# Kernel optimization log

Hardware: AMD Instinct MI355X
Metric: run time of the kernel (lower is better)

The kernel has to match this reference:

```python
import jax, jax.numpy as jnp
import numpy as np

N_HEAD = 12

def fillnan(x):
    return jnp.nan_to_num(x, nan=0.0, posinf=0.0, neginf=0.0)

def setup_inputs() -> dict:
    key = jax.random.key(0)
    k1, k2, k3 = jax.random.split(key, 3)
    B, T, C = 2, 2048, 768
    x = jax.random.normal(k1, (B, T, C), dtype=jnp.float32)
    W_attn = jax.random.normal(k2, (3 * C, C), dtype=jnp.float32) * 0.02
    W_proj = jax.random.normal(k3, (C, C), dtype=jnp.float32) * 0.02
    return {"x": x, "W_attn": W_attn, "W_proj": W_proj}

def reference(x, W_attn, W_proj):
    B, T, C = x.shape
    H = N_HEAD
    D = C // H
    # qkv projection (torch Linear: x @ W^T), then nan-sanitize
    qkv = fillnan(jnp.einsum('btc,fc->btf', x, W_attn))  # [B,T,3C]
    q, k, v = jnp.split(qkv, 3, axis=-1)
    # [B,T,C] -> [B,H,T,D]
    q = q.reshape(B, T, H, D).transpose(0, 2, 1, 3)
    k = k.reshape(B, T, H, D).transpose(0, 2, 1, 3)
    v = v.reshape(B, T, H, D).transpose(0, 2, 1, 3)
    scale = 1.0 / np.sqrt(D).astype(np.float32)
    att = jnp.einsum('bhqd,bhkd->bhqk', q, k) * scale  # [B,H,T,T]
    att = fillnan(att)
    causal = jnp.tril(jnp.ones((T, T), dtype=bool))
    att = jnp.where(causal[None, None], att, -jnp.inf)
    att = jax.nn.softmax(att, axis=-1)
    att = fillnan(att)
    y = jnp.einsum('bhqk,bhkd->bhqd', att, v)  # [B,H,T,D]
    y = fillnan(y)
    y = y.transpose(0, 2, 1, 3).reshape(B, T, C)
    y = fillnan(jnp.einsum('btc,fc->btf', y, W_proj))
    return y
```

## Files before the change

### kernel.cpp

```cpp
#include <hip/hip_runtime.h>

typedef __attribute__((ext_vector_type(8))) short bf16x8;
typedef __attribute__((ext_vector_type(4))) float f32x4;

__device__ __forceinline__ unsigned short f2b(float f) {
  union { float f; unsigned u; } v; v.f = f;
  return (unsigned short)((v.u + 0x7FFFu + ((v.u >> 16) & 1u)) >> 16);
}
__device__ __forceinline__ unsigned short f2b_fast(float f) {
  union { float f; unsigned u; } v; v.f = f;
  return (unsigned short)((v.u + 0x8000u) >> 16);
}

#define XN4   786432
#define WAN4  442368
#define WPN4  147456
__global__ void cvt_all(const float* __restrict__ x, const float* __restrict__ Wa,
                        const float* __restrict__ Wp,
                        unsigned short* __restrict__ xb, unsigned short* __restrict__ Wab,
                        unsigned short* __restrict__ Wpb) {
  int i = blockIdx.x * 256 + threadIdx.x;
  const float* src; unsigned short* dst; int off;
  if (i < XN4)            { src = x;  dst = xb;  off = i; }
  else if (i < XN4 + WAN4){ src = Wa; dst = Wab; off = i - XN4; }
  else                    { src = Wp; dst = Wpb; off = i - XN4 - WAN4; }
  float4 f = reinterpret_cast<const float4*>(src)[off];
  ushort4 o;
  o.x = f2b(f.x); o.y = f2b(f.y); o.z = f2b(f.z); o.w = f2b(f.w);
  reinterpret_cast<ushort4*>(dst)[off] = o;
}

#define BM 128
#define BN 128
#define BK 64

__global__ __launch_bounds__(256, 2)
void gemm_nt(const unsigned short* __restrict__ A,
             const unsigned short* __restrict__ Bm,
             int M, int N, int K, int mode,
             unsigned short* __restrict__ qb,
             unsigned short* __restrict__ kb_,
             unsigned short* __restrict__ vt,
             float* __restrict__ outf) {
  __shared__ unsigned short As[BM * BK];
  __shared__ unsigned short Bs[BN * BK];
  int tid = threadIdx.x;
  int wave = tid >> 6, lane = tid & 63;
  int quad = lane >> 4, l16 = lane & 15;
  int m0 = blockIdx.x * BM, n0 = blockIdx.y * BN;
  int wm = (wave & 1) * 64, wn = (wave >> 1) * 64;

  int srow = lane >> 3;
  int scol = ((lane & 7) ^ srow) << 3;

  f32x4 acc[4][4] = {};

  for (int k0 = 0; k0 < K; k0 += BK) {
    __syncthreads();
#pragma unroll
    for (int i = 0; i < 4; ++i) {
      int r = wave * 32 + i * 8;
      __builtin_amdgcn_global_load_lds(
          (const __attribute__((address_space(1))) unsigned int*)(A + (size_t)(m0 + r + srow) * K + k0 + scol),
          (__attribute__((address_space(3))) unsigned int*)(As + r * BK), 16, 0, 0);
      __builtin_amdgcn_global_load_lds(
          (const __attribute__((address_space(1))) unsigned int*)(Bm + (size_t)(n0 + r + srow) * K + k0 + scol),
          (__attribute__((address_space(3))) unsigned int*)(Bs + r * BK), 16, 0, 0);
    }
    __syncthreads();
#pragma unroll
    for (int kb = 0; kb < 2; ++kb) {
      int ch = (((kb << 2) | quad) ^ (l16 & 7)) << 3;
      bf16x8 af[4], bf[4];
#pragma unroll
      for (int i = 0; i < 4; ++i)
        af[i] = *reinterpret_cast<const bf16x8*>(As + (wm + i * 16 + l16) * BK + ch);
#pragma unroll
      for (int j = 0; j < 4; ++j)
        bf[j] = *reinterpret_cast<const bf16x8*>(Bs + (wn + j * 16 + l16) * BK + ch);
#pragma unroll
      for (int i = 0; i < 4; ++i)
#pragma unroll
        for (int j = 0; j < 4; ++j)
          acc[i][j] = __builtin_amdgcn_mfma_f32_16x16x32_bf16(af[i], bf[j], acc[i][j], 0, 0, 0);
    }
  }

  const float scale2 = 0.125f * 1.44269504089f;
#pragma unroll
  for (int i = 0; i < 4; ++i) {
    int mbase = m0 + wm + i * 16 + quad * 4;
#pragma unroll
    for (int j = 0; j < 4; ++j) {
      int f = n0 + wn + j * 16 + l16;
#pragma unroll
      for (int r = 0; r < 4; ++r) {
        float c = acc[i][j][r];
        int m = mbase + r;
        if (mode == 0) {
          int b = m >> 11, t = m & 2047;
          int which = f / 768;
          int f2 = f - which * 768;
          int h = f2 >> 6, d = f2 & 63;
          int bh = b * 12 + h;
          if (which == 0)      qb[((size_t)(bh * 2048 + t)) * 64 + d] = f2b(c * scale2);
          else if (which == 1) kb_[((size_t)(bh * 2048 + t)) * 64 + d] = f2b(c);
          else                 vt[((size_t)(bh * 64 + d)) * 2048 + t] = f2b(c);
        } else {
          outf[(size_t)m * N + f] = c;
        }
      }
    }
  }
}

#define PLDP 72

__global__ __launch_bounds__(256, 4)
void attn_part(const unsigned short* __restrict__ Qb,
               const unsigned short* __restrict__ Kb,
               const unsigned short* __restrict__ Vt,
               float* __restrict__ Oacc, float* __restrict__ Lacc) {
  __shared__ unsigned short Ks[64 * 64];
  __shared__ unsigned short Vs[64 * 64];
  __shared__ unsigned short P[4 * 32 * PLDP];
  const int T = 2048, D = 64;
  int wave = threadIdx.x >> 6, lane = threadIdx.x & 63;
  int quad = lane >> 4, l16 = lane & 15;

  int w = blockIdx.x;
  int bh = w / 72;
  int r = w - bh * 72;
  int b = 0;
#pragma unroll
  for (int i = 0; i < 16; ++i) {
    int nb = (i >> 1) + 1;
    if (r >= nb) { r -= nb; b = i + 1; } else break;
  }
  int c = r;
  int q0 = b * 128;
  int qrow = q0 + wave * 32;
  int kbeg = c * 256;
  int kend = kbeg + 256; if (kend > q0 + 128) kend = q0 + 128;

  const unsigned short* Qp = Qb + (size_t)bh * T * D;
  const unsigned short* Kp = Kb + (size_t)bh * T * D;
  const unsigned short* Vp = Vt + (size_t)bh * D * T;
  unsigned short* Pw = P + wave * 32 * PLDP;

  int srow = lane >> 3;
  int scol = ((lane & 7) ^ srow) << 3;

  bf16x8 aq[2][2];
#pragma unroll
  for (int qi = 0; qi < 2; ++qi)
#pragma unroll
    for (int cc = 0; cc < 2; ++cc)
      aq[qi][cc] = *reinterpret_cast<const bf16x8*>(
          Qp + (qrow + qi * 16 + l16) * D + cc * 32 + quad * 8);

  bf16x8 ones;
#pragma unroll
  for (int e = 0; e < 8; ++e) ones[e] = (short)0x3F80;

  f32x4 o[2][4] = {};
  f32x4 lacc[2] = {};

  for (int k0 = kbeg; k0 < kend; k0 += 64) {
    __syncthreads();
#pragma unroll
    for (int i = 0; i < 2; ++i) {
      int rr = wave * 16 + i * 8;
      __builtin_amdgcn_global_load_lds(
          (const __attribute__((address_space(1))) unsigned int*)(Kp + (size_t)(k0 + rr + srow) * D + scol),
          (__attribute__((address_space(3))) unsigned int*)(Ks + rr * 64), 16, 0, 0);
      __builtin_amdgcn_global_load_lds(
          (const __attribute__((address_space(1))) unsigned int*)(Vp + (size_t)(rr + srow) * T + k0 + scol),
          (__attribute__((address_space(3))) unsigned int*)(Vs + rr * 64), 16, 0, 0);
    }
    __syncthreads();

    if (k0 > qrow + 31) continue;

    f32x4 sacc[2][4] = {};
#pragma unroll
    for (int nt = 0; nt < 4; ++nt) {
      bf16x8 bk0 = *reinterpret_cast<const bf16x8*>(Ks + (nt * 16 + l16) * 64 + ((quad ^ (l16 & 7)) << 3));
      bf16x8 bk1 = *reinterpret_cast<const bf16x8*>(Ks + (nt * 16 + l16) * 64 + (((4 | quad) ^ (l16 & 7)) << 3));
#pragma unroll
      for (int qi = 0; qi < 2; ++qi) {
        sacc[qi][nt] = __builtin_amdgcn_mfma_f32_16x16x32_bf16(aq[qi][0], bk0, sacc[qi][nt], 0, 0, 0);
        sacc[qi][nt] = __builtin_amdgcn_mfma_f32_16x16x32_bf16(aq[qi][1], bk1, sacc[qi][nt], 0, 0, 0);
      }
    }

    if (k0 + 63 > qrow) {
#pragma unroll
      for (int qi = 0; qi < 2; ++qi)
#pragma unroll
        for (int nt = 0; nt < 4; ++nt) {
          int col = k0 + nt * 16 + l16;
#pragma unroll
          for (int rr = 0; rr < 4; ++rr) {
            int row = qrow + qi * 16 + quad * 4 + rr;
            sacc[qi][nt][rr] = (col <= row) ? sacc[qi][nt][rr] : -1e30f;
          }
        }
    }
#pragma unroll
    for (int qi = 0; qi < 2; ++qi)
#pragma unroll
      for (int nt = 0; nt < 4; ++nt)
#pragma unroll
        for (int rr = 0; rr < 4; ++rr)
          sacc[qi][nt][rr] = exp2f(sacc[qi][nt][rr]);

#pragma unroll
    for (int qi = 0; qi < 2; ++qi)
#pragma unroll
      for (int nt = 0; nt < 4; ++nt)
#pragma unroll
        for (int rr = 0; rr < 4; ++rr)
          Pw[(qi * 16 + quad * 4 + rr) * PLDP + nt * 16 + l16] = f2b_fast(sacc[qi][nt][rr]);
    __asm__ volatile("s_waitcnt lgkmcnt(0)" ::: "memory");

    bf16x8 vf[4][2];
#pragma unroll
    for (int dt = 0; dt < 4; ++dt) {
      vf[dt][0] = *reinterpret_cast<const bf16x8*>(Vs + (dt * 16 + l16) * 64 + ((quad ^ (l16 & 7)) << 3));
      vf[dt][1] = *reinterpret_cast<const bf16x8*>(Vs + (dt * 16 + l16) * 64 + (((4 | quad) ^ (l16 & 7)) << 3));
    }
#pragma unroll
    for (int qi = 0; qi < 2; ++qi) {
      bf16x8 ap0 = *reinterpret_cast<const bf16x8*>(Pw + (qi * 16 + l16) * PLDP + quad * 8);
      bf16x8 ap1 = *reinterpret_cast<const bf16x8*>(Pw + (qi * 16 + l16) * PLDP + 32 + quad * 8);
#pragma unroll
      for (int dt = 0; dt < 4; ++dt) {
        o[qi][dt] = __builtin_amdgcn_mfma_f32_16x16x32_bf16(ap0, vf[dt][0], o[qi][dt], 0, 0, 0);
        o[qi][dt] = __builtin_amdgcn_mfma_f32_16x16x32_bf16(ap1, vf[dt][1], o[qi][dt], 0, 0, 0);
      }
      lacc[qi] = __builtin_amdgcn_mfma_f32_16x16x32_bf16(ap0, ones, lacc[qi], 0, 0, 0);
      lacc[qi] = __builtin_amdgcn_mfma_f32_16x16x32_bf16(ap1, ones, lacc[qi], 0, 0, 0);
    }
  }

#pragma unroll
  for (int qi = 0; qi < 2; ++qi)
#pragma unroll
    for (int dt = 0; dt < 4; ++dt)
#pragma unroll
      for (int rr = 0; rr < 4; ++rr) {
        int row = qrow + qi * 16 + quad * 4 + rr;
        atomicAdd(&Oacc[((size_t)(bh * T + row)) * 64 + dt * 16 + l16], o[qi][dt][rr]);
      }
  if (l16 == 0) {
#pragma unroll
    for (int qi = 0; qi < 2; ++qi)
#pragma unroll
      for (int rr = 0; rr < 4; ++rr)
        atomicAdd(&Lacc[bh * T + qrow + qi * 16 + quad * 4 + rr], lacc[qi][rr]);
  }
}

__global__ __launch_bounds__(256)
void attn_norm(const float* __restrict__ Oacc, const float* __restrict__ Lacc,
               unsigned short* __restrict__ Yb) {
  int g = blockIdx.x * 256 + threadIdx.x;
  int d4 = g & 15;
  int t = (g >> 4) & 2047;
  int bh = g >> 15;
  int b = bh / 12, h = bh - b * 12;
  float4 ov = reinterpret_cast<const float4*>(Oacc)[g];
  float rl = 1.0f / Lacc[bh * 2048 + t];
  ushort4 y;
  y.x = f2b(ov.x * rl); y.y = f2b(ov.y * rl);
  y.z = f2b(ov.z * rl); y.w = f2b(ov.w * rl);
  *reinterpret_cast<ushort4*>(Yb + ((size_t)(b * 2048 + t)) * 768 + h * 64 + d4 * 4) = y;
}

extern "C" void kernel_launch(void* const* d_in, const int* in_sizes, int n_in,
                              void* d_out, int out_size, void* d_ws, size_t ws_size,
                              hipStream_t stream) {
  const float* x  = (const float*)d_in[0];
  const float* Wa = (const float*)d_in[1];
  const float* Wp = (const float*)d_in[2];
  float* out = (float*)d_out;

  unsigned short* ws = (unsigned short*)d_ws;
  unsigned short* xb  = ws;
  unsigned short* Wab = xb  + 3145728;
  unsigned short* Wpb = Wab + 1769472;
  unsigned short* Qb  = Wpb + 589824;
  unsigned short* Kb  = Qb  + 3145728;
  unsigned short* Vt  = Kb  + 3145728;
  unsigned short* Yb  = Vt  + 3145728;
  float*          Oacc = (float*)(Yb + 3145728);
  float*          Lacc = Oacc + 3145728;

  hipMemsetAsync(Oacc, 0, (3145728 + 49152) * sizeof(float), stream);

  cvt_all<<<(XN4 + WAN4 + WPN4) / 256, 256, 0, stream>>>(x, Wa, Wp, xb, Wab, Wpb);

  gemm_nt<<<dim3(4096 / BM, 2304 / BN), 256, 0, stream>>>(
      xb, Wab, 4096, 2304, 768, 0, Qb, Kb, Vt, nullptr);

  attn_part<<<1728, 256, 0, stream>>>(Qb, Kb, Vt, Oacc, Lacc);
  attn_norm<<<786432 / 256, 256, 0, stream>>>(Oacc, Lacc, Yb);

  gemm_nt<<<dim3(4096 / BM, 768 / BN), 256, 0, stream>>>(
      Yb, Wpb, 4096, 768, 768, 1, nullptr, nullptr, nullptr, out);
}
```

Measured before the change: 178.8 us.

## Replace split-K attention with per-query-block kernel, double-buffered KV and fused normalization

Each block now handles one 128-row query block across the full causal key range for a head. The old design split keys across blocks, accumulated partials with atomics into fp32 buffers and then ran a separate normalize kernel. K/V tiles are double-buffered in LDS so the next tile's loads overlap compute, and MFMA sections get raised wave priority. This removes the memset, the atomics and the extra kernel launch, but the grid shrinks to 384 blocks with unbalanced causal work (scheduled heaviest first) and occupancy drops to 2 blocks per CU.

```diff
diff --git a/kernel.cpp b/kernel.cpp
--- a/kernel.cpp
+++ b/kernel.cpp
@@ -116,32 +116,23 @@
 
 #define PLDP 72
 
-__global__ __launch_bounds__(256, 4)
+__global__ __launch_bounds__(256, 2)
 void attn_part(const unsigned short* __restrict__ Qb,
                const unsigned short* __restrict__ Kb,
                const unsigned short* __restrict__ Vt,
-               float* __restrict__ Oacc, float* __restrict__ Lacc) {
-  __shared__ unsigned short Ks[64 * 64];
-  __shared__ unsigned short Vs[64 * 64];
+               unsigned short* __restrict__ Yb) {
+  __shared__ unsigned short Ks[2][64 * 64];
+  __shared__ unsigned short Vs[2][64 * 64];
   __shared__ unsigned short P[4 * 32 * PLDP];
   const int T = 2048, D = 64;
   int wave = threadIdx.x >> 6, lane = threadIdx.x & 63;
   int quad = lane >> 4, l16 = lane & 15;
 
-  int w = blockIdx.x;
-  int bh = w / 72;
-  int r = w - bh * 72;
-  int b = 0;
-#pragma unroll
-  for (int i = 0; i < 16; ++i) {
-    int nb = (i >> 1) + 1;
-    if (r >= nb) { r -= nb; b = i + 1; } else break;
-  }
-  int c = r;
-  int q0 = b * 128;
+  int bh = blockIdx.x % 24;
+  int qb = 15 - blockIdx.x / 24;
+  int q0 = qb * 128;
   int qrow = q0 + wave * 32;
-  int kbeg = c * 256;
-  int kend = kbeg + 256; if (kend > q0 + 128) kend = q0 + 128;
+  int nt = 2 * qb + 2;
 
   const unsigned short* Qp = Qb + (size_t)bh * T * D;
   const unsigned short* Kp = Kb + (size_t)bh * T * D;
@@ -166,116 +157,113 @@
   f32x4 o[2][4] = {};
   f32x4 lacc[2] = {};
 
-  for (int k0 = kbeg; k0 < kend; k0 += 64) {
-    __syncthreads();
-#pragma unroll
-    for (int i = 0; i < 2; ++i) {
-      int rr = wave * 16 + i * 8;
-      __builtin_amdgcn_global_load_lds(
-          (const __attribute__((address_space(1))) unsigned int*)(Kp + (size_t)(k0 + rr + srow) * D + scol),
-          (__attribute__((address_space(3))) unsigned int*)(Ks + rr * 64), 16, 0, 0);
-      __builtin_amdgcn_global_load_lds(
-          (const __attribute__((address_space(1))) unsigned int*)(Vp + (size_t)(rr + srow) * T + k0 + scol),
-          (__attribute__((address_space(3))) unsigned int*)(Vs + rr * 64), 16, 0, 0);
-    }
-    __syncthreads();
-
-    if (k0 > qrow + 31) continue;
-
-    f32x4 sacc[2][4] = {};
-#pragma unroll
-    for (int nt = 0; nt < 4; ++nt) {
-      bf16x8 bk0 = *reinterpret_cast<const bf16x8*>(Ks + (nt * 16 + l16) * 64 + ((quad ^ (l16 & 7)) << 3));
-      bf16x8 bk1 = *reinterpret_cast<const bf16x8*>(Ks + (nt * 16 + l16) * 64 + (((4 | quad) ^ (l16 & 7)) << 3));
+#define STAGE_KV(buf, k0s)                                                          \
+  {                                                                                 \
+    _Pragma("unroll")                                                               \
+    for (int i_ = 0; i_ < 2; ++i_) {                                                \
+      int rr_ = wave * 16 + i_ * 8;                                                 \
+      __builtin_amdgcn_global_load_lds(                                             \
+          (const __attribute__((address_space(1))) unsigned int*)(Kp + (size_t)((k0s) + rr_ + srow) * 64 + scol), \
+          (__attribute__((address_space(3))) unsigned int*)(&Ks[buf][rr_ * 64]), 16, 0, 0); \
+      __builtin_amdgcn_global_load_lds(                                             \
+          (const __attribute__((address_space(1))) unsigned int*)(Vp + (size_t)(rr_ + srow) * 2048 + (k0s) + scol), \
+          (__attribute__((address_space(3))) unsigned int*)(&Vs[buf][rr_ * 64]), 16, 0, 0); \
+    }                                                                               \
+  }
+
+  STAGE_KV(0, 0);
+  asm volatile("s_waitcnt vmcnt(0)" ::: "memory");
+  __builtin_amdgcn_s_barrier();
+
+  int cur = 0;
+  for (int t = 0; t < nt; ++t) {
+    int k0 = t << 6;
+    if (t + 1 < nt) STAGE_KV(cur ^ 1, (t + 1) << 6);
+
+    if (k0 <= qrow + 31) {
+      f32x4 sacc[2][4] = {};
+      __builtin_amdgcn_s_setprio(1);
+#pragma unroll
+      for (int nt2 = 0; nt2 < 4; ++nt2) {
+        bf16x8 bk0 = *reinterpret_cast<const bf16x8*>(Ks[cur] + (nt2 * 16 + l16) * 64 + ((quad ^ (l16 & 7)) << 3));
+        bf16x8 bk1 = *reinterpret_cast<const bf16x8*>(Ks[cur] + (nt2 * 16 + l16) * 64 + (((4 | quad) ^ (l16 & 7)) << 3));
+#pragma unroll
+        for (int qi = 0; qi < 2; ++qi) {
+          sacc[qi][nt2] = __builtin_amdgcn_mfma_f32_16x16x32_bf16(aq[qi][0], bk0, sacc[qi][nt2], 0, 0, 0);
+          sacc[qi][nt2] = __builtin_amdgcn_mfma_f32_16x16x32_bf16(aq[qi][1], bk1, sacc[qi][nt2], 0, 0, 0);
+        }
+      }
+      __builtin_amdgcn_s_setprio(0);
+
+      if (k0 + 63 > qrow) {
+#pragma unroll
+        for (int qi = 0; qi < 2; ++qi)
+#pragma unroll
+          for (int nt2 = 0; nt2 < 4; ++nt2) {
+            int col = k0 + nt2 * 16 + l16;
+#pragma unroll
+            for (int rr = 0; rr < 4; ++rr) {
+              int row = qrow + qi * 16 + quad * 4 + rr;
+              sacc[qi][nt2][rr] = (col <= row) ? sacc[qi][nt2][rr] : -1e30f;
+            }
+          }
+      }
+#pragma unroll
+      for (int qi = 0; qi < 2; ++qi)
+#pragma unroll
+        for (int nt2 = 0; nt2 < 4; ++nt2)
+#pragma unroll
+          for (int rr = 0; rr < 4; ++rr)
+            sacc[qi][nt2][rr] = exp2f(sacc[qi][nt2][rr]);
+
+#pragma unroll
+      for (int qi = 0; qi < 2; ++qi)
+#pragma unroll
+        for (int nt2 = 0; nt2 < 4; ++nt2)
+#pragma unroll
+          for (int rr = 0; rr < 4; ++rr)
+            Pw[(qi * 16 + quad * 4 + rr) * PLDP + nt2 * 16 + l16] = f2b_fast(sacc[qi][nt2][rr]);
+      __asm__ volatile("s_waitcnt lgkmcnt(0)" ::: "memory");
+
+      bf16x8 vf[4][2];
+#pragma unroll
+      for (int dt = 0; dt < 4; ++dt) {
+        vf[dt][0] = *reinterpret_cast<const bf16x8*>(Vs[cur] + (dt * 16 + l16) * 64 + ((quad ^ (l16 & 7)) << 3));
+        vf[dt][1] = *reinterpret_cast<const bf16x8*>(Vs[cur] + (dt * 16 + l16) * 64 + (((4 | quad) ^ (l16 & 7)) << 3));
+      }
+      __builtin_amdgcn_s_setprio(1);
 #pragma unroll
       for (int qi = 0; qi < 2; ++qi) {
-        sacc[qi][nt] = __builtin_amdgcn_mfma_f32_16x16x32_bf16(aq[qi][0], bk0, sacc[qi][nt], 0, 0, 0);
-        sacc[qi][nt] = __builtin_amdgcn_mfma_f32_16x16x32_bf16(aq[qi][1], bk1, sacc[qi][nt], 0, 0, 0);
-      }
-    }
-
-    if (k0 + 63 > qrow) {
-#pragma unroll
-      for (int qi = 0; qi < 2; ++qi)
-#pragma unroll
-        for (int nt = 0; nt < 4; ++nt) {
-          int col = k0 + nt * 16 + l16;
-#pragma unroll
-          for (int rr = 0; rr < 4; ++rr) {
-            int row = qrow + qi * 16 + quad * 4 + rr;
-            sacc[qi][nt][rr] = (col <= row) ? sacc[qi][nt][rr] : -1e30f;
-          }
+        bf16x8 ap0 = *reinterpret_cast<const bf16x8*>(Pw + (qi * 16 + l16) * PLDP + quad * 8);
+        bf16x8 ap1 = *reinterpret_cast<const bf16x8*>(Pw + (qi * 16 + l16) * PLDP + 32 + quad * 8);
+#pragma unroll
+        for (int dt = 0; dt < 4; ++dt) {
+          o[qi][dt] = __builtin_amdgcn_mfma_f32_16x16x32_bf16(ap0, vf[dt][0], o[qi][dt], 0, 0, 0);
+          o[qi][dt] = __builtin_amdgcn_mfma_f32_16x16x32_bf16(ap1, vf[dt][1], o[qi][dt], 0, 0, 0);
         }
-    }
-#pragma unroll
-    for (int qi = 0; qi < 2; ++qi)
-#pragma unroll
-      for (int nt = 0; nt < 4; ++nt)
-#pragma unroll
-        for (int rr = 0; rr < 4; ++rr)
-          sacc[qi][nt][rr] = exp2f(sacc[qi][nt][rr]);
-
-#pragma unroll
-    for (int qi = 0; qi < 2; ++qi)
-#pragma unroll
-      for (int nt = 0; nt < 4; ++nt)
-#pragma unroll
-        for (int rr = 0; rr < 4; ++rr)
-          Pw[(qi * 16 + quad * 4 + rr) * PLDP + nt * 16 + l16] = f2b_fast(sacc[qi][nt][rr]);
-    __asm__ volatile("s_waitcnt lgkmcnt(0)" ::: "memory");
-
-    bf16x8 vf[4][2];
-#pragma unroll
-    for (int dt = 0; dt < 4; ++dt) {
-      vf[dt][0] = *reinterpret_cast<const bf16x8*>(Vs + (dt * 16 + l16) * 64 + ((quad ^ (l16 & 7)) << 3));
-      vf[dt][1] = *reinterpret_cast<const bf16x8*>(Vs + (dt * 16 + l16) * 64 + (((4 | quad) ^ (l16 & 7)) << 3));
-    }
-#pragma unroll
-    for (int qi = 0; qi < 2; ++qi) {
-      bf16x8 ap0 = *reinterpret_cast<const bf16x8*>(Pw + (qi * 16 + l16) * PLDP + quad * 8);
-      bf16x8 ap1 = *reinterpret_cast<const bf16x8*>(Pw + (qi * 16 + l16) * PLDP + 32 + quad * 8);
-#pragma unroll
-      for (int dt = 0; dt < 4; ++dt) {
-        o[qi][dt] = __builtin_amdgcn_mfma_f32_16x16x32_bf16(ap0, vf[dt][0], o[qi][dt], 0, 0, 0);
-        o[qi][dt] = __builtin_amdgcn_mfma_f32_16x16x32_bf16(ap1, vf[dt][1], o[qi][dt], 0, 0, 0);
-      }
-      lacc[qi] = __builtin_amdgcn_mfma_f32_16x16x32_bf16(ap0, ones, lacc[qi], 0, 0, 0);
-      lacc[qi] = __builtin_amdgcn_mfma_f32_16x16x32_bf16(ap1, ones, lacc[qi], 0, 0, 0);
-    }
-  }
-
+        lacc[qi] = __builtin_amdgcn_mfma_f32_16x16x32_bf16(ap0, ones, lacc[qi], 0, 0, 0);
+        lacc[qi] = __builtin_amdgcn_mfma_f32_16x16x32_bf16(ap1, ones, lacc[qi], 0, 0, 0);
+      }
+      __builtin_amdgcn_s_setprio(0);
+    }
+
+    asm volatile("s_waitcnt vmcnt(0)" ::: "memory");
+    __builtin_amdgcn_s_barrier();
+    cur ^= 1;
+  }
+
+  int b = bh / 12, h = bh - b * 12;
+  unsigned short* Yw = Yb + (size_t)b * 2048 * 768 + h * 64;
 #pragma unroll
   for (int qi = 0; qi < 2; ++qi)
 #pragma unroll
-    for (int dt = 0; dt < 4; ++dt)
-#pragma unroll
-      for (int rr = 0; rr < 4; ++rr) {
-        int row = qrow + qi * 16 + quad * 4 + rr;
-        atomicAdd(&Oacc[((size_t)(bh * T + row)) * 64 + dt * 16 + l16], o[qi][dt][rr]);
-      }
-  if (l16 == 0) {
-#pragma unroll
-    for (int qi = 0; qi < 2; ++qi)
-#pragma unroll
-      for (int rr = 0; rr < 4; ++rr)
-        atomicAdd(&Lacc[bh * T + qrow + qi * 16 + quad * 4 + rr], lacc[qi][rr]);
-  }
-}
-
-__global__ __launch_bounds__(256)
-void attn_norm(const float* __restrict__ Oacc, const float* __restrict__ Lacc,
-               unsigned short* __restrict__ Yb) {
-  int g = blockIdx.x * 256 + threadIdx.x;
-  int d4 = g & 15;
-  int t = (g >> 4) & 2047;
-  int bh = g >> 15;
-  int b = bh / 12, h = bh - b * 12;
-  float4 ov = reinterpret_cast<const float4*>(Oacc)[g];
-  float rl = 1.0f / Lacc[bh * 2048 + t];
-  ushort4 y;
-  y.x = f2b(ov.x * rl); y.y = f2b(ov.y * rl);
-  y.z = f2b(ov.z * rl); y.w = f2b(ov.w * rl);
-  *reinterpret_cast<ushort4*>(Yb + ((size_t)(b * 2048 + t)) * 768 + h * 64 + d4 * 4) = y;
+    for (int rr = 0; rr < 4; ++rr) {
+      int row = qrow + qi * 16 + quad * 4 + rr;
+      float rl = 1.0f / lacc[qi][rr];
+#pragma unroll
+      for (int dt = 0; dt < 4; ++dt)
+        Yw[(size_t)row * 768 + dt * 16 + l16] = f2b(o[qi][dt][rr] * rl);
+    }
 }
 
 extern "C" void kernel_launch(void* const* d_in, const int* in_sizes, int n_in,
@@ -294,18 +282,13 @@
   unsigned short* Kb  = Qb  + 3145728;
   unsigned short* Vt  = Kb  + 3145728;
   unsigned short* Yb  = Vt  + 3145728;
-  float*          Oacc = (float*)(Yb + 3145728);
-  float*          Lacc = Oacc + 3145728;
-
-  hipMemsetAsync(Oacc, 0, (3145728 + 49152) * sizeof(float), stream);
 
   cvt_all<<<(XN4 + WAN4 + WPN4) / 256, 256, 0, stream>>>(x, Wa, Wp, xb, Wab, Wpb);
 
   gemm_nt<<<dim3(4096 / BM, 2304 / BN), 256, 0, stream>>>(
       xb, Wab, 4096, 2304, 768, 0, Qb, Kb, Vt, nullptr);
 
-  attn_part<<<1728, 256, 0, stream>>>(Qb, Kb, Vt, Oacc, Lacc);
-  attn_norm<<<786432 / 256, 256, 0, stream>>>(Oacc, Lacc, Yb);
+  attn_part<<<384, 256, 0, stream>>>(Qb, Kb, Vt, Yb);
 
   gemm_nt<<<dim3(4096 / BM, 768 / BN), 256, 0, stream>>>(
       Yb, Wpb, 4096, 768, 768, 1, nullptr, nullptr, nullptr, out);
```

Result: faster. 166.2 us (-7.1%).
